# Performance work log

Measured on AMD Instinct MI355X. Metric: run time of the kernel, lower is better.

Reference implementation:

```python
import jax, jax.numpy as jnp
import numpy as np

NQ = 8
DIM = 2 ** NQ  # 256
PAIRS = [(i, j) for i in range(NQ) for j in range(i + 1, NQ)]
CNOT = jnp.array([[1, 0, 0, 0], [0, 1, 0, 0], [0, 0, 0, 1], [0, 0, 1, 0]], jnp.complex64)


def rx(t):
    c = jnp.cos(t / 2).astype(jnp.complex64)
    s = (-1j * jnp.sin(t / 2)).astype(jnp.complex64)
    return jnp.stack([jnp.stack([c, s]), jnp.stack([s, c])])


def ry(t):
    c = jnp.cos(t / 2)
    s = jnp.sin(t / 2)
    return jnp.stack([jnp.stack([c, -s]), jnp.stack([s, c])]).astype(jnp.complex64)


def rz(t):
    e = jnp.exp(-1j * jnp.asarray(t, jnp.float32) / 2).astype(jnp.complex64)
    z = jnp.zeros((), jnp.complex64)
    return jnp.stack([jnp.stack([e, z]), jnp.stack([z, jnp.conj(e)])])


def ising_xx(phi):
    c = jnp.cos(phi / 2).astype(jnp.complex64)
    s = (-1j * jnp.sin(phi / 2)).astype(jnp.complex64)
    z = jnp.zeros((), jnp.complex64)
    return jnp.stack([
        jnp.stack([c, z, z, s]),
        jnp.stack([z, c, s, z]),
        jnp.stack([z, s, c, z]),
        jnp.stack([s, z, z, c]),
    ])


def apply_u(rho, U, wires):
    """rho: (2,)*16 tensor (8 ket axes, 8 bra axes). Apply U rho U^dagger on wires."""
    k = len(wires)
    Ut = U.reshape((2,) * (2 * k))
    rho = jnp.tensordot(Ut, rho, axes=(tuple(range(k, 2 * k)), tuple(wires)))
    rho = jnp.moveaxis(rho, tuple(range(k)), tuple(wires))
    bra = tuple(w + NQ for w in wires)
    rho = jnp.tensordot(jnp.conj(Ut), rho, axes=(tuple(range(k, 2 * k)), bra))
    rho = jnp.moveaxis(rho, tuple(range(k)), bra)
    return rho


def conv_block(rho, b1, b2, p):
    rho = apply_u(rho, rz(-jnp.pi / 2), (b2,))
    rho = apply_u(rho, CNOT, (b2, b1))
    rho = apply_u(rho, rz(p[0]), (b1,))
    rho = apply_u(rho, ry(p[1]), (b2,))
    rho = apply_u(rho, CNOT, (b1, b2))
    rho = apply_u(rho, ry(p[2]), (b2,))
    rho = apply_u(rho, CNOT, (b2, b1))
    rho = apply_u(rho, rz(jnp.pi / 2), (b1,))
    return rho


def pool_block(rho, b1, b2, p):
    rho = apply_u(rho, rz(-jnp.pi / 2), (b2,))
    rho = apply_u(rho, CNOT, (b2, b1))
    rho = apply_u(rho, rz(p[0]), (b1,))
    rho = apply_u(rho, ry(p[1]), (b2,))
    rho = apply_u(rho, CNOT, (b1, b2))
    rho = apply_u(rho, ry(p[2]), (b2,))
    return rho


def quantum_fusion_layer(x, weights, coupling, p_flip):
    # AmplitudeEmbedding with normalize=True -> pure state, then rho = |psi><psi|
    psi = (x / jnp.sqrt(jnp.sum(x * x))).astype(jnp.complex64)
    rho = jnp.outer(psi, jnp.conj(psi)).reshape((2,) * (2 * NQ))
    X = jnp.array([[0, 1], [1, 0]], jnp.complex64)
    for i in range(NQ):
        rho = apply_u(rho, rx(weights[i]), (i,))
        rho = apply_u(rho, ry(weights[i + NQ]), (i,))
        rho = apply_u(rho, rz(weights[i + 2 * NQ]), (i,))
        if p_flip > 0.0:  # BitFlip channel; identity when p=0
            rho = (1.0 - p_flip) * rho + p_flip * apply_u(rho, X, (i,))
    for (i, j) in PAIRS:
        rho = apply_u(rho, ising_xx(coupling[i, j]), (i, j))
    # data-dependent adjacency -> blend (equivalent to conditional apply for adj in {0,1})
    cmin = coupling.min()
    cmax = coupling.max()
    adj = ((coupling - cmin) / (cmax - cmin)) > 0.5
    count = jnp.zeros((), jnp.int32)
    for (i, j) in PAIRS:
        a = adj[i, j]
        idx = 3 * NQ + 6 * count
        p6 = jax.lax.dynamic_slice(weights, (idx,), (6,))
        r2 = conv_block(rho, i, j, p6[:3])
        r2 = pool_block(r2, i, j, p6[3:])
        af = a.astype(jnp.float32)
        rho = af * r2 + (1.0 - af) * rho
        count = count + a.astype(jnp.int32)
    return rho.reshape(DIM, DIM)


def setup_inputs() -> dict:
    key = jax.random.key(0)
    k1, k2, k3 = jax.random.split(key, 3)
    x = jax.random.uniform(k1, (DIM,), dtype=jnp.float32)
    weights = jax.random.uniform(k2, (210,), dtype=jnp.float32)
    coupling = jax.random.uniform(k3, (NQ, NQ), dtype=jnp.float32)
    return {"x": x, "weights": weights, "coupling": coupling}


def reference(x, weights, coupling):
    # forward returns the noiseless state (noise_strength=0); the noisy run is only printed
    return quantum_fusion_layer(x, weights, coupling, 0.0)
```

## Files before the change

kernel.cpp:

```cpp
#include <hip/hip_runtime.h>

#define RHALF 0.70710678118654752440f
#define INV2PI 0.15915494309189535f

typedef float2 cpx;

static __device__ __forceinline__ cpx cmul(cpx a, cpx b) {
    return make_float2(a.x*b.x - a.y*b.y, a.x*b.y + a.y*b.x);
}
static __device__ __forceinline__ void cmac(cpx& n, cpx k, cpx a) {
    n.x += k.x*a.x - k.y*a.y;
    n.y += k.x*a.y + k.y*a.x;
}

static __device__ __forceinline__ void fsc(float a, float& s, float& c) {
    float r = a * INV2PI;
    s = __builtin_amdgcn_sinf(r);
    c = __builtin_amdgcn_cosf(r);
}

struct St { float vr[4]; float vi[4]; int lane; };

static __device__ __forceinline__ void xxupd(float& ar, float& ai, float pr, float pi, float c, float s) {
    ar = c*ar + s*pi;
    ai = c*ai - s*pr;
}

static __device__ __forceinline__ void xx2(float& ar,float& ai,float& br,float& bi,int lm,float c,float s) {
    float pbr = __shfl_xor(ar, lm, 64), pbi = __shfl_xor(ai, lm, 64);
    float par = __shfl_xor(br, lm, 64), pai = __shfl_xor(bi, lm, 64);
    xxupd(ar,ai,par,pai,c,s);
    xxupd(br,bi,pbr,pbi,c,s);
}


static __device__ __forceinline__ void gXX(St& st, int qa, int qb, float c, float s) {
    if (qb <= 1) {
        float p0r=st.vr[3],p0i=st.vi[3],p1r=st.vr[2],p1i=st.vi[2];
        float p2r=st.vr[1],p2i=st.vi[1],p3r=st.vr[0],p3i=st.vi[0];
        xxupd(st.vr[0],st.vi[0],p0r,p0i,c,s);
        xxupd(st.vr[1],st.vi[1],p1r,p1i,c,s);
        xxupd(st.vr[2],st.vi[2],p2r,p2i,c,s);
        xxupd(st.vr[3],st.vi[3],p3r,p3i,c,s);
    } else if (qa <= 1) {
        int lm = 1 << (7-qb);
        if (qa == 0) {
            xx2(st.vr[0],st.vi[0],st.vr[2],st.vi[2],lm,c,s);
            xx2(st.vr[1],st.vi[1],st.vr[3],st.vi[3],lm,c,s);
        } else {
            xx2(st.vr[0],st.vi[0],st.vr[1],st.vi[1],lm,c,s);
            xx2(st.vr[2],st.vi[2],st.vr[3],st.vi[3],lm,c,s);
        }
    } else {
        int lm = (1<<(7-qa)) | (1<<(7-qb));
        #pragma unroll
        for (int k=0;k<4;++k) {
            float pr = __shfl_xor(st.vr[k], lm, 64);
            float pi = __shfl_xor(st.vi[k], lm, 64);
            xxupd(st.vr[k],st.vi[k],pr,pi,c,s);
        }
    }
}


static __device__ __forceinline__ void applyBlockLL(St& st, const cpx* bm, int p, int i, int j) {
    int mi = 1 << (7-i), mj = 1 << (7-j);
    int r = ((st.lane & mi) ? 2 : 0) | ((st.lane & mj) ? 1 : 0);
    const cpx* row = bm + p*16 + r*4;
    cpx K0 = row[r], K1 = row[r^1], K2 = row[r^2], K3 = row[r^3];
    #pragma unroll
    for (int k=0;k<4;++k) {
        float p1r = __shfl_xor(st.vr[k], mj, 64),    p1i = __shfl_xor(st.vi[k], mj, 64);
        float p2r = __shfl_xor(st.vr[k], mi, 64),    p2i = __shfl_xor(st.vi[k], mi, 64);
        float p3r = __shfl_xor(st.vr[k], mi|mj, 64), p3i = __shfl_xor(st.vi[k], mi|mj, 64);
        cpx n = make_float2(0.f,0.f);
        cmac(n, K0, make_float2(st.vr[k], st.vi[k]));
        cmac(n, K1, make_float2(p1r,p1i));
        cmac(n, K2, make_float2(p2r,p2i));
        cmac(n, K3, make_float2(p3r,p3i));
        st.vr[k] = n.x; st.vi[k] = n.y;
    }
}

static __device__ __forceinline__ void applyBlockMixed(St& st, const cpx* bm, int p, int i, int j) {
    int mj = 1 << (7-j);
    int bj = (st.lane & mj) ? 1 : 0;
    const cpx* base = bm + p*16;
    cpx lo0 = base[bj*4+0], lo1 = base[bj*4+1], lo2 = base[bj*4+2], lo3 = base[bj*4+3];
    cpx hi0 = base[(2+bj)*4+0], hi1 = base[(2+bj)*4+1], hi2 = base[(2+bj)*4+2], hi3 = base[(2+bj)*4+3];
    cpx lo_o0 = bj ? lo1 : lo0;  cpx lo_s0 = bj ? lo0 : lo1;
    cpx lo_o1 = bj ? lo3 : lo2;  cpx lo_s1 = bj ? lo2 : lo3;
    cpx hi_o0 = bj ? hi1 : hi0;  cpx hi_s0 = bj ? hi0 : hi1;
    cpx hi_o1 = bj ? hi3 : hi2;  cpx hi_s1 = bj ? hi2 : hi3;
    float sr[4], si[4];
    #pragma unroll
    for (int k=0;k<4;++k) { sr[k] = __shfl_xor(st.vr[k], mj, 64); si[k] = __shfl_xor(st.vi[k], mj, 64); }
    int ri = (i==0) ? 2 : 1;
    #pragma unroll
    for (int t=0; t<2; ++t) {
        int k0 = (i==0) ? t : (t*2);
        int k1 = k0 | ri;
        cpx a0 = make_float2(st.vr[k0], st.vi[k0]);
        cpx a1 = make_float2(st.vr[k1], st.vi[k1]);
        cpx s0 = make_float2(sr[k0], si[k0]);
        cpx s1 = make_float2(sr[k1], si[k1]);
        cpx n0 = make_float2(0.f,0.f), n1 = make_float2(0.f,0.f);
        cmac(n0, lo_o0, a0); cmac(n0, lo_s0, s0); cmac(n0, lo_o1, a1); cmac(n0, lo_s1, s1);
        cmac(n1, hi_o0, a0); cmac(n1, hi_s0, s0); cmac(n1, hi_o1, a1); cmac(n1, hi_s1, s1);
        st.vr[k0]=n0.x; st.vi[k0]=n0.y; st.vr[k1]=n1.x; st.vi[k1]=n1.y;
    }
}

static __device__ __forceinline__ void applyBlock01(St& st, const cpx* bm, int p) {
    const cpx* base = bm + p*16;
    cpx a[4];
    #pragma unroll
    for (int k=0;k<4;++k) a[k] = make_float2(st.vr[k], st.vi[k]);
    #pragma unroll
    for (int r=0;r<4;++r) {
        cpx n = make_float2(0.f,0.f);
        #pragma unroll
        for (int c=0;c<4;++c) cmac(n, base[r*4+c], a[c]);
        st.vr[r]=n.x; st.vi[r]=n.y;
    }
}

__global__ __launch_bounds__(64) void evolve_kernel(const float* __restrict__ x,
                                                    const float* __restrict__ w,
                                                    const float* __restrict__ cp,
                                                    float2* __restrict__ psi) {
    __shared__ float wsh[256];
    __shared__ cpx tc[64];
    __shared__ cpx u1[32];
    __shared__ cpx bmat[28*16];
    int lane = threadIdx.x;

    float xv[4], wv[4];
    #pragma unroll
    for (int k=0;k<4;++k) {
        int idx = k*64 + lane;
        xv[k] = x[idx];
        wv[k] = (idx < 210) ? w[idx] : 0.0f;
    }
    float cv = cp[lane];
    #pragma unroll
    for (int k=0;k<4;++k) wsh[k*64+lane] = wv[k];

    St st; st.lane = lane;
    float ss = 0.f;
    #pragma unroll
    for (int k=0;k<4;++k) { st.vr[k] = xv[k]; st.vi[k] = 0.f; ss += xv[k]*xv[k]; }
    #pragma unroll
    for (int m=32;m>0;m>>=1) ss += __shfl_xor(ss, m, 64);
    float inv = 1.0f / sqrtf(ss);
    #pragma unroll
    for (int k=0;k<4;++k) st.vr[k] *= inv;

    { float sn, cn; fsc(0.5f*cv, sn, cn); tc[lane] = make_float2(cn, sn); }
    float mn = cv, mx = cv;
    #pragma unroll
    for (int m=32;m>0;m>>=1) {
        mn = fminf(mn, __shfl_xor(mn, m, 64));
        mx = fmaxf(mx, __shfl_xor(mx, m, 64));
    }
    unsigned long long adj64 = __ballot(((cv - mn) / (mx - mn)) > 0.5f);

    int ii = 0, jj = 0;
    if (lane < 28) {
        int rem = lane;
        while (rem >= 7-ii) { rem -= 7-ii; ++ii; }
        jj = ii + 1 + rem;
    }
    unsigned int f = (lane < 28) ? (unsigned int)((adj64 >> (ii*8 + jj)) & 1ull) : 0u;
    unsigned long long pmw = __ballot(f != 0u);
    unsigned int pm = (unsigned int)(pmw & 0xFFFFFFFull);
    int prefix = __popcll(pmw & ((1ull << lane) - 1ull));

    __syncthreads();

    if (lane < 8) {
        int q = lane;
        float sn0,cn0,sn1,cn1,sn2,cn2;
        fsc(0.5f*wsh[q],    sn0, cn0);
        fsc(0.5f*wsh[q+8],  sn1, cn1);
        fsc(0.5f*wsh[q+16], sn2, cn2);
        cpx A00 = make_float2( cn1*cn0,  sn1*sn0);
        cpx A01 = make_float2(-sn1*cn0, -cn1*sn0);
        cpx A10 = make_float2( sn1*cn0, -cn1*sn0);
        cpx A11 = make_float2( cn1*cn0, -sn1*sn0);
        cpx e0 = make_float2(cn2,-sn2), e1 = make_float2(cn2, sn2);
        u1[q*4+0] = cmul(e0,A00); u1[q*4+1] = cmul(e0,A01);
        u1[q*4+2] = cmul(e1,A10); u1[q*4+3] = cmul(e1,A11);
    }

    if (lane < 28) {
        int idx = 24 + 6*prefix;
        float s0,c0,s1,c1,s2,c2,s3,c3,s4,c4,s5,c5;
        fsc(0.5f*wsh[idx+0], s0, c0);
        fsc(0.5f*wsh[idx+1], s1, c1);
        fsc(0.5f*wsh[idx+2], s2, c2);
        fsc(0.5f*wsh[idx+3], s3, c3);
        fsc(0.5f*wsh[idx+4], s4, c4);
        fsc(0.5f*wsh[idx+5], s5, c5);
        cpx m[16];
        #pragma unroll
        for (int e=0;e<16;++e) m[e] = make_float2(0.f,0.f);
        m[0]  = make_float2(RHALF,  RHALF);
        m[5]  = make_float2(RHALF, -RHALF);
        m[10] = make_float2(RHALF,  RHALF);
        m[15] = make_float2(RHALF, -RHALF);
        #define RSWAP(a,b) { _Pragma("unroll") for (int c_=0;c_<4;++c_){ cpx t_=m[(a)*4+c_]; m[(a)*4+c_]=m[(b)*4+c_]; m[(b)*4+c_]=t_; } }
        #define DIAG_I(e0x,e0y,e1x,e1y) { cpx ea_=make_float2(e0x,e0y), eb_=make_float2(e1x,e1y); \
            _Pragma("unroll") for (int e_=0;e_<8;++e_)  m[e_]   = cmul(ea_, m[e_]); \
            _Pragma("unroll") for (int e_=8;e_<16;++e_) m[e_]   = cmul(eb_, m[e_]); }
        #define DIAG_J(e0x,e0y,e1x,e1y) { cpx ea_=make_float2(e0x,e0y), eb_=make_float2(e1x,e1y); \
            _Pragma("unroll") for (int c_=0;c_<4;++c_){ m[c_]=cmul(ea_,m[c_]); m[8+c_]=cmul(ea_,m[8+c_]); \
                                                        m[4+c_]=cmul(eb_,m[4+c_]); m[12+c_]=cmul(eb_,m[12+c_]); } }
        #define RY_J(cc,sc) { _Pragma("unroll") for (int c_=0;c_<4;++c_){ \
            cpx a_=m[c_],   b_=m[4+c_];  m[c_]  =make_float2((cc)*a_.x-(sc)*b_.x,(cc)*a_.y-(sc)*b_.y); \
                                         m[4+c_]=make_float2((sc)*a_.x+(cc)*b_.x,(sc)*a_.y+(cc)*b_.y); \
            cpx d_=m[8+c_], e_=m[12+c_]; m[8+c_] =make_float2((cc)*d_.x-(sc)*e_.x,(cc)*d_.y-(sc)*e_.y); \
                                         m[12+c_]=make_float2((sc)*d_.x+(cc)*e_.x,(sc)*d_.y+(cc)*e_.y); } }
        RSWAP(1,3)
        DIAG_I(c0,-s0, c0, s0)
        RY_J(c1,s1)
        RSWAP(2,3)
        RY_J(c2,s2)
        RSWAP(1,3)
        DIAG_I(RHALF,-RHALF, RHALF,RHALF)
        DIAG_J(RHALF,RHALF, RHALF,-RHALF)
        RSWAP(1,3)
        DIAG_I(c3,-s3, c3, s3)
        RY_J(c4,s4)
        RSWAP(2,3)
        RY_J(c5,s5)
        #pragma unroll
        for (int e=0;e<16;++e) bmat[lane*16+e] = m[e];
        #undef RSWAP
        #undef DIAG_I
        #undef DIAG_J
        #undef RY_J
    }

    __syncthreads();

    #pragma unroll
    for (int q=0;q<8;++q) {
        cpx U00=u1[q*4+0], U01=u1[q*4+1], U10=u1[q*4+2], U11=u1[q*4+3];
        if (q >= 2) {
            int ml = 1 << (7-q);
            bool hi = (lane & ml) != 0;
            cpx A = hi ? U11 : U00;
            cpx B = hi ? U10 : U01;
            #pragma unroll
            for (int k=0;k<4;++k) {
                float pr = __shfl_xor(st.vr[k], ml, 64);
                float pi = __shfl_xor(st.vi[k], ml, 64);
                cpx n = make_float2(0.f,0.f);
                cmac(n, A, make_float2(st.vr[k], st.vi[k]));
                cmac(n, B, make_float2(pr, pi));
                st.vr[k]=n.x; st.vi[k]=n.y;
            }
        } else {
            int ri = (q==0) ? 2 : 1;
            #pragma unroll
            for (int t=0;t<2;++t) {
                int k0 = (q==0) ? t : (t*2);
                int k1 = k0 | ri;
                cpx a = make_float2(st.vr[k0], st.vi[k0]);
                cpx b = make_float2(st.vr[k1], st.vi[k1]);
                cpx n0 = make_float2(0.f,0.f), n1 = make_float2(0.f,0.f);
                cmac(n0, U00, a); cmac(n0, U01, b);
                cmac(n1, U10, a); cmac(n1, U11, b);
                st.vr[k0]=n0.x; st.vi[k0]=n0.y; st.vr[k1]=n1.x; st.vi[k1]=n1.y;
            }
        }
    }

    {
        constexpr int XI[28] = {0,1,2,3, 1,0,3,4, 2,1,0,5, 3,2,1,0, 4,3,2,0, 5,4,0,1, 6,0,1,2};
        constexpr int XJ[28] = {7,6,5,4, 7,2,6,5, 7,3,4,6, 7,4,5,6, 7,5,6,1, 7,6,3,2, 7,5,4,3};
        cpx csx[28];
        #pragma unroll
        for (int g=0; g<28; ++g) csx[g] = tc[XI[g]*8 + XJ[g]];
        #pragma unroll
        for (int g=0; g<28; ++g) gXX(st, XI[g], XJ[g], csx[g].x, csx[g].y);
    }

    {
        constexpr int PI3[28] = {0,0,0,0,0,0,0, 1,1,1,1,1,1, 2,2,2,2,2, 3,3,3,3, 4,4,4, 5,5, 6};
        constexpr int PJ3[28] = {1,2,3,4,5,6,7, 2,3,4,5,6,7, 3,4,5,6,7, 4,5,6,7, 5,6,7, 6,7, 7};
        #pragma unroll
        for (int p=0;p<28;++p) {
            if ((pm >> p) & 1u) {
                const int i = PI3[p], j = PJ3[p];
                if (i >= 2)      applyBlockLL(st, bmat, p, i, j);
                else if (j >= 2) applyBlockMixed(st, bmat, p, i, j);
                else             applyBlock01(st, bmat, p);
            }
        }
    }

    #pragma unroll
    for (int k=0;k<4;++k) psi[k*64+lane] = make_float2(st.vr[k], st.vi[k]);
}

__global__ __launch_bounds__(256) void outer_planar(const float2* __restrict__ psi,
                                                    float* __restrict__ out) {
    int c = threadIdx.x;
    int r = blockIdx.x;
    float2 pr = psi[r];
    float2 pc = psi[c];
    int idx = (r<<8) + c;
    out[idx]         = pr.x*pc.x + pr.y*pc.y;
    out[idx + 65536] = pr.y*pc.x - pr.x*pc.y;
}

__global__ __launch_bounds__(256) void outer_real(const float2* __restrict__ psi,
                                                  float* __restrict__ out) {
    int c = threadIdx.x;
    int r = blockIdx.x;
    float2 pr = psi[r];
    float2 pc = psi[c];
    out[(r<<8) + c] = pr.x*pc.x + pr.y*pc.y;
}

__global__ __launch_bounds__(256) void outer_interleaved(const float2* __restrict__ psi,
                                                         float2* __restrict__ out) {
    int c = threadIdx.x;
    int r = blockIdx.x;
    float2 pr = psi[r];
    float2 pc = psi[c];
    out[(r<<8) + c] = make_float2(pr.x*pc.x + pr.y*pc.y, pr.y*pc.x - pr.x*pc.y);
}

extern "C" void kernel_launch(void* const* d_in, const int* in_sizes, int n_in,
                              void* d_out, int out_size, void* d_ws, size_t ws_size,
                              hipStream_t stream) {
    (void)in_sizes; (void)n_in; (void)ws_size;
    const float* x  = (const float*)d_in[0];
    const float* w  = (const float*)d_in[1];
    const float* cp = (const float*)d_in[2];
    float2* psi = (float2*)d_ws;
    hipLaunchKernelGGL(evolve_kernel, dim3(1), dim3(64), 0, stream, x, w, cp, psi);
    if (out_size == 65536) {
        hipLaunchKernelGGL(outer_real, dim3(256), dim3(256), 0, stream, psi, (float*)d_out);
    } else if (out_size == 131072) {
        hipLaunchKernelGGL(outer_planar, dim3(256), dim3(256), 0, stream, psi, (float*)d_out);
    } else {
        hipLaunchKernelGGL(outer_interleaved, dim3(256), dim3(256), 0, stream, psi, (float2*)d_out);
    }
}
```

Baseline: 67.74 us.

## Fuse state evolution into outer-product kernel with redundant per-block recompute

For the planar output, the separate single-block evolve kernel and the outer-product kernel become one launch of 256 single-wave blocks. Each block recomputes the full 256-amplitude state evolution redundantly, stages it in shared memory, then writes one row of the density matrix with float4 stores. This removes a kernel launch and the global round trip of the state vector, at the cost of 256x redundant evolve work spread across CUs. The complex multiply-accumulate chains are also split into two partial accumulators to shorten dependency chains.

```diff
diff --git a/kernel.cpp b/kernel.cpp
--- a/kernel.cpp
+++ b/kernel.cpp
@@ -20,6 +20,13 @@
 }
 
 struct St { float vr[4]; float vi[4]; int lane; };
+
+struct SharedBufs {
+    float wsh[256];
+    cpx   tc[64];
+    cpx   u1[32];
+    cpx   bmat[448];
+};
 
 static __device__ __forceinline__ void xxupd(float& ar, float& ai, float pr, float pi, float c, float s) {
     ar = c*ar + s*pi;
@@ -73,12 +80,12 @@
         float p1r = __shfl_xor(st.vr[k], mj, 64),    p1i = __shfl_xor(st.vi[k], mj, 64);
         float p2r = __shfl_xor(st.vr[k], mi, 64),    p2i = __shfl_xor(st.vi[k], mi, 64);
         float p3r = __shfl_xor(st.vr[k], mi|mj, 64), p3i = __shfl_xor(st.vi[k], mi|mj, 64);
-        cpx n = make_float2(0.f,0.f);
-        cmac(n, K0, make_float2(st.vr[k], st.vi[k]));
-        cmac(n, K1, make_float2(p1r,p1i));
-        cmac(n, K2, make_float2(p2r,p2i));
-        cmac(n, K3, make_float2(p3r,p3i));
-        st.vr[k] = n.x; st.vi[k] = n.y;
+        cpx n1 = make_float2(0.f,0.f), n2 = make_float2(0.f,0.f);
+        cmac(n1, K0, make_float2(st.vr[k], st.vi[k]));
+        cmac(n1, K1, make_float2(p1r,p1i));
+        cmac(n2, K2, make_float2(p2r,p2i));
+        cmac(n2, K3, make_float2(p3r,p3i));
+        st.vr[k] = n1.x + n2.x; st.vi[k] = n1.y + n2.y;
     }
 }
 
@@ -104,10 +111,14 @@
         cpx a1 = make_float2(st.vr[k1], st.vi[k1]);
         cpx s0 = make_float2(sr[k0], si[k0]);
         cpx s1 = make_float2(sr[k1], si[k1]);
-        cpx n0 = make_float2(0.f,0.f), n1 = make_float2(0.f,0.f);
-        cmac(n0, lo_o0, a0); cmac(n0, lo_s0, s0); cmac(n0, lo_o1, a1); cmac(n0, lo_s1, s1);
-        cmac(n1, hi_o0, a0); cmac(n1, hi_s0, s0); cmac(n1, hi_o1, a1); cmac(n1, hi_s1, s1);
-        st.vr[k0]=n0.x; st.vi[k0]=n0.y; st.vr[k1]=n1.x; st.vi[k1]=n1.y;
+        cpx n0a = make_float2(0.f,0.f), n0b = make_float2(0.f,0.f);
+        cpx n1a = make_float2(0.f,0.f), n1b = make_float2(0.f,0.f);
+        cmac(n0a, lo_o0, a0); cmac(n0a, lo_s0, s0);
+        cmac(n0b, lo_o1, a1); cmac(n0b, lo_s1, s1);
+        cmac(n1a, hi_o0, a0); cmac(n1a, hi_s0, s0);
+        cmac(n1b, hi_o1, a1); cmac(n1b, hi_s1, s1);
+        st.vr[k0]=n0a.x+n0b.x; st.vi[k0]=n0a.y+n0b.y;
+        st.vr[k1]=n1a.x+n1b.x; st.vi[k1]=n1a.y+n1b.y;
     }
 }
 
@@ -118,22 +129,18 @@
     for (int k=0;k<4;++k) a[k] = make_float2(st.vr[k], st.vi[k]);
     #pragma unroll
     for (int r=0;r<4;++r) {
-        cpx n = make_float2(0.f,0.f);
-        #pragma unroll
-        for (int c=0;c<4;++c) cmac(n, base[r*4+c], a[c]);
-        st.vr[r]=n.x; st.vi[r]=n.y;
-    }
-}
-
-__global__ __launch_bounds__(64) void evolve_kernel(const float* __restrict__ x,
-                                                    const float* __restrict__ w,
-                                                    const float* __restrict__ cp,
-                                                    float2* __restrict__ psi) {
-    __shared__ float wsh[256];
-    __shared__ cpx tc[64];
-    __shared__ cpx u1[32];
-    __shared__ cpx bmat[28*16];
-    int lane = threadIdx.x;
+        cpx n1 = make_float2(0.f,0.f), n2 = make_float2(0.f,0.f);
+        cmac(n1, base[r*4+0], a[0]); cmac(n1, base[r*4+1], a[1]);
+        cmac(n2, base[r*4+2], a[2]); cmac(n2, base[r*4+3], a[3]);
+        st.vr[r]=n1.x+n2.x; st.vi[r]=n1.y+n2.y;
+    }
+}
+
+static __device__ __forceinline__ void evolve_body(const float* __restrict__ x,
+                                                   const float* __restrict__ w,
+                                                   const float* __restrict__ cp,
+                                                   SharedBufs& sh, St& st) {
+    int lane = st.lane;
 
     float xv[4], wv[4];
     #pragma unroll
@@ -144,9 +151,8 @@
     }
     float cv = cp[lane];
     #pragma unroll
-    for (int k=0;k<4;++k) wsh[k*64+lane] = wv[k];
-
-    St st; st.lane = lane;
+    for (int k=0;k<4;++k) sh.wsh[k*64+lane] = wv[k];
+
     float ss = 0.f;
     #pragma unroll
     for (int k=0;k<4;++k) { st.vr[k] = xv[k]; st.vi[k] = 0.f; ss += xv[k]*xv[k]; }
@@ -156,7 +162,7 @@
     #pragma unroll
     for (int k=0;k<4;++k) st.vr[k] *= inv;
 
-    { float sn, cn; fsc(0.5f*cv, sn, cn); tc[lane] = make_float2(cn, sn); }
+    { float sn, cn; fsc(0.5f*cv, sn, cn); sh.tc[lane] = make_float2(cn, sn); }
     float mn = cv, mx = cv;
     #pragma unroll
     for (int m=32;m>0;m>>=1) {
@@ -181,27 +187,27 @@
     if (lane < 8) {
         int q = lane;
         float sn0,cn0,sn1,cn1,sn2,cn2;
-        fsc(0.5f*wsh[q],    sn0, cn0);
-        fsc(0.5f*wsh[q+8],  sn1, cn1);
-        fsc(0.5f*wsh[q+16], sn2, cn2);
+        fsc(0.5f*sh.wsh[q],    sn0, cn0);
+        fsc(0.5f*sh.wsh[q+8],  sn1, cn1);
+        fsc(0.5f*sh.wsh[q+16], sn2, cn2);
         cpx A00 = make_float2( cn1*cn0,  sn1*sn0);
         cpx A01 = make_float2(-sn1*cn0, -cn1*sn0);
         cpx A10 = make_float2( sn1*cn0, -cn1*sn0);
         cpx A11 = make_float2( cn1*cn0, -sn1*sn0);
         cpx e0 = make_float2(cn2,-sn2), e1 = make_float2(cn2, sn2);
-        u1[q*4+0] = cmul(e0,A00); u1[q*4+1] = cmul(e0,A01);
-        u1[q*4+2] = cmul(e1,A10); u1[q*4+3] = cmul(e1,A11);
+        sh.u1[q*4+0] = cmul(e0,A00); sh.u1[q*4+1] = cmul(e0,A01);
+        sh.u1[q*4+2] = cmul(e1,A10); sh.u1[q*4+3] = cmul(e1,A11);
     }
 
     if (lane < 28) {
         int idx = 24 + 6*prefix;
         float s0,c0,s1,c1,s2,c2,s3,c3,s4,c4,s5,c5;
-        fsc(0.5f*wsh[idx+0], s0, c0);
-        fsc(0.5f*wsh[idx+1], s1, c1);
-        fsc(0.5f*wsh[idx+2], s2, c2);
-        fsc(0.5f*wsh[idx+3], s3, c3);
-        fsc(0.5f*wsh[idx+4], s4, c4);
-        fsc(0.5f*wsh[idx+5], s5, c5);
+        fsc(0.5f*sh.wsh[idx+0], s0, c0);
+        fsc(0.5f*sh.wsh[idx+1], s1, c1);
+        fsc(0.5f*sh.wsh[idx+2], s2, c2);
+        fsc(0.5f*sh.wsh[idx+3], s3, c3);
+        fsc(0.5f*sh.wsh[idx+4], s4, c4);
+        fsc(0.5f*sh.wsh[idx+5], s5, c5);
         cpx m[16];
         #pragma unroll
         for (int e=0;e<16;++e) m[e] = make_float2(0.f,0.f);
@@ -235,7 +241,7 @@
         RSWAP(2,3)
         RY_J(c5,s5)
         #pragma unroll
-        for (int e=0;e<16;++e) bmat[lane*16+e] = m[e];
+        for (int e=0;e<16;++e) sh.bmat[lane*16+e] = m[e];
         #undef RSWAP
         #undef DIAG_I
         #undef DIAG_J
@@ -246,7 +252,7 @@
 
     #pragma unroll
     for (int q=0;q<8;++q) {
-        cpx U00=u1[q*4+0], U01=u1[q*4+1], U10=u1[q*4+2], U11=u1[q*4+3];
+        cpx U00=sh.u1[q*4+0], U01=sh.u1[q*4+1], U10=sh.u1[q*4+2], U11=sh.u1[q*4+3];
         if (q >= 2) {
             int ml = 1 << (7-q);
             bool hi = (lane & ml) != 0;
@@ -282,7 +288,7 @@
         constexpr int XJ[28] = {7,6,5,4, 7,2,6,5, 7,3,4,6, 7,4,5,6, 7,5,6,1, 7,6,3,2, 7,5,4,3};
         cpx csx[28];
         #pragma unroll
-        for (int g=0; g<28; ++g) csx[g] = tc[XI[g]*8 + XJ[g]];
+        for (int g=0; g<28; ++g) csx[g] = sh.tc[XI[g]*8 + XJ[g]];
         #pragma unroll
         for (int g=0; g<28; ++g) gXX(st, XI[g], XJ[g], csx[g].x, csx[g].y);
     }
@@ -294,26 +300,46 @@
         for (int p=0;p<28;++p) {
             if ((pm >> p) & 1u) {
                 const int i = PI3[p], j = PJ3[p];
-                if (i >= 2)      applyBlockLL(st, bmat, p, i, j);
-                else if (j >= 2) applyBlockMixed(st, bmat, p, i, j);
-                else             applyBlock01(st, bmat, p);
+                if (i >= 2)      applyBlockLL(st, sh.bmat, p, i, j);
+                else if (j >= 2) applyBlockMixed(st, sh.bmat, p, i, j);
+                else             applyBlock01(st, sh.bmat, p);
             }
         }
     }
-
-    #pragma unroll
-    for (int k=0;k<4;++k) psi[k*64+lane] = make_float2(st.vr[k], st.vi[k]);
-}
-
-__global__ __launch_bounds__(256) void outer_planar(const float2* __restrict__ psi,
-                                                    float* __restrict__ out) {
-    int c = threadIdx.x;
+}
+
+__global__ __launch_bounds__(64) void fused_planar(const float* __restrict__ x,
+                                                   const float* __restrict__ w,
+                                                   const float* __restrict__ cp,
+                                                   float* __restrict__ out) {
+    __shared__ SharedBufs sh;
+    __shared__ cpx ps[256];
+    St st; st.lane = threadIdx.x;
+    evolve_body(x, w, cp, sh, st);
+    int lane = st.lane;
+    #pragma unroll
+    for (int k=0;k<4;++k) ps[k*64+lane] = make_float2(st.vr[k], st.vi[k]);
+    __syncthreads();
     int r = blockIdx.x;
-    float2 pr = psi[r];
-    float2 pc = psi[c];
-    int idx = (r<<8) + c;
-    out[idx]         = pr.x*pc.x + pr.y*pc.y;
-    out[idx + 65536] = pr.y*pc.x - pr.x*pc.y;
+    cpx pr = ps[r];
+    cpx c0 = ps[4*lane+0], c1 = ps[4*lane+1], c2 = ps[4*lane+2], c3 = ps[4*lane+3];
+    float4 re = make_float4(pr.x*c0.x + pr.y*c0.y, pr.x*c1.x + pr.y*c1.y,
+                            pr.x*c2.x + pr.y*c2.y, pr.x*c3.x + pr.y*c3.y);
+    float4 im = make_float4(pr.y*c0.x - pr.x*c0.y, pr.y*c1.x - pr.x*c1.y,
+                            pr.y*c2.x - pr.x*c2.y, pr.y*c3.x - pr.x*c3.y);
+    ((float4*)(out + (r<<8)))[lane] = re;
+    ((float4*)(out + 65536 + (r<<8)))[lane] = im;
+}
+
+__global__ __launch_bounds__(64) void evolve_kernel(const float* __restrict__ x,
+                                                    const float* __restrict__ w,
+                                                    const float* __restrict__ cp,
+                                                    float2* __restrict__ psi) {
+    __shared__ SharedBufs sh;
+    St st; st.lane = threadIdx.x;
+    evolve_body(x, w, cp, sh, st);
+    #pragma unroll
+    for (int k=0;k<4;++k) psi[k*64+st.lane] = make_float2(st.vr[k], st.vi[k]);
 }
 
 __global__ __launch_bounds__(256) void outer_real(const float2* __restrict__ psi,
@@ -341,13 +367,15 @@
     const float* x  = (const float*)d_in[0];
     const float* w  = (const float*)d_in[1];
     const float* cp = (const float*)d_in[2];
-    float2* psi = (float2*)d_ws;
-    hipLaunchKernelGGL(evolve_kernel, dim3(1), dim3(64), 0, stream, x, w, cp, psi);
-    if (out_size == 65536) {
-        hipLaunchKernelGGL(outer_real, dim3(256), dim3(256), 0, stream, psi, (float*)d_out);
-    } else if (out_size == 131072) {
-        hipLaunchKernelGGL(outer_planar, dim3(256), dim3(256), 0, stream, psi, (float*)d_out);
+    if (out_size == 131072) {
+        hipLaunchKernelGGL(fused_planar, dim3(256), dim3(64), 0, stream, x, w, cp, (float*)d_out);
     } else {
-        hipLaunchKernelGGL(outer_interleaved, dim3(256), dim3(256), 0, stream, psi, (float2*)d_out);
-    }
-}
+        float2* psi = (float2*)d_ws;
+        hipLaunchKernelGGL(evolve_kernel, dim3(1), dim3(64), 0, stream, x, w, cp, psi);
+        if (out_size == 65536) {
+            hipLaunchKernelGGL(outer_real, dim3(256), dim3(256), 0, stream, psi, (float*)d_out);
+        } else {
+            hipLaunchKernelGGL(outer_interleaved, dim3(256), dim3(256), 0, stream, psi, (float2*)d_out);
+        }
+    }
+}
```

New measurement: 67.98 us. About the same (+0.3%).
